# Optimization experiments

Hardware: AMD Instinct MI355X
Metric: run time of the kernel (lower is better)

## Reference

```python
import jax, jax.numpy as jnp
import numpy as np

B, T, IN_DIM, EMB = 8, 2048, 1024, 1024
NEG_INF = -1e30  # stand-in for float('-inf'); exp() underflows to 0 identically


def setup_inputs() -> dict:
    key = jax.random.key(0)
    ks = jax.random.split(key, 7)
    s = 1.0 / np.sqrt(IN_DIM)
    return {
        "x": jax.random.normal(ks[0], (B, T, IN_DIM), dtype=jnp.float32),
        "Wq": jax.random.normal(ks[1], (IN_DIM, EMB), dtype=jnp.float32) * s,
        "bq": jax.random.normal(ks[2], (EMB,), dtype=jnp.float32) * 0.01,
        "Wk": jax.random.normal(ks[3], (IN_DIM, EMB), dtype=jnp.float32) * s,
        "bk": jax.random.normal(ks[4], (EMB,), dtype=jnp.float32) * 0.01,
        "Wv": jax.random.normal(ks[5], (IN_DIM, EMB), dtype=jnp.float32) * s,
        "bv": jax.random.normal(ks[6], (EMB,), dtype=jnp.float32) * 0.01,
    }


def reference(x, Wq, bq, Wk, bk, Wv, bv):
    # projections: [B, T, EMB]
    q = x @ Wq + bq
    k = x @ Wk + bk
    v = x @ Wv + bv
    scale = jnp.asarray(EMB, x.dtype) ** 0.5
    # scores: [B, T, T]
    scores = jnp.einsum("btd,bsd->bts", q, k) / scale
    Tq = scores.shape[-2]
    causal = jnp.tril(jnp.ones((Tq, Tq), dtype=bool))  # [T, T]
    scores = jnp.where(causal, scores, jnp.asarray(NEG_INF, scores.dtype))
    # Faithful to torch.vmap(softmax): per-batch GLOBAL-matrix softmax
    # (max and sum taken over the whole [T, T] matrix, not per row).
    m = jnp.max(scores, axis=(-2, -1), keepdims=True)
    e = jnp.exp(scores - m)
    w = e / jnp.sum(e, axis=(-2, -1), keepdims=True)
    # output: [B, T, EMB]
    return jnp.einsum("bts,bsd->btd", w, v)
```

## Files before the change

### kernel.cpp

```cpp
#include <hip/hip_runtime.h>
#include <stdint.h>


#define B_   8
#define T_   2048
#define DIM  1024

typedef _Float16 f16;
typedef f16   f16x8 __attribute__((ext_vector_type(8)));
typedef f16   f16x4 __attribute__((ext_vector_type(4)));
typedef float f32x4 __attribute__((ext_vector_type(4)));

typedef const __attribute__((address_space(1))) void gvoid_t;
typedef __attribute__((address_space(3))) void lvoid_t;


__device__ __forceinline__ void stage_half256(const uint16_t* __restrict__ g, int ld,
                                              uint16_t* s, int tid) {
#pragma unroll
  for (int j = 0; j < 2; ++j) {
    int r   = j * 64 + (tid >> 3);
    int seg = (tid & 7) ^ (r & 7);
    const uint16_t* gp = g + (size_t)r * ld + seg * 8;
    uint16_t* sp = s + j * 4096 + (tid >> 6) * 512;
    __builtin_amdgcn_global_load_lds((gvoid_t*)gp, (lvoid_t*)sp, 16, 0, 0);
  }
}

__device__ __forceinline__ f16x8 frag64(const uint16_t* s, int r, int gseg) {
  return *(const f16x8*)(s + r * 64 + ((gseg ^ (r & 7)) * 8));
}

__device__ __forceinline__ void lda4(const uint16_t* s, int rbase, int quad, int l15,
                                     f16x8 o[4][2]) {
#pragma unroll
  for (int mf = 0; mf < 4; ++mf) {
    int r = rbase + mf * 16 + l15;
#pragma unroll
    for (int kk = 0; kk < 2; ++kk) o[mf][kk] = frag64(s, r, kk * 4 + quad);
  }
}

__device__ __forceinline__ void ldb2(const uint16_t* s, int rbase, int quad, int l15,
                                     f16x8 o[2][2]) {
#pragma unroll
  for (int nf = 0; nf < 2; ++nf) {
    int r = rbase + nf * 16 + l15;
#pragma unroll
    for (int kk = 0; kk < 2; ++kk) o[nf][kk] = frag64(s, r, kk * 4 + quad);
  }
}

template <int M0, int N0>
__device__ __forceinline__ void mm16(f16x8 a[4][2], f16x8 b[2][2], f32x4 (&acc)[8][4]) {
#pragma unroll
  for (int kk = 0; kk < 2; ++kk)
#pragma unroll
    for (int mf = 0; mf < 4; ++mf)
#pragma unroll
      for (int nf = 0; nf < 2; ++nf)
        acc[M0 + mf][N0 + nf] = __builtin_amdgcn_mfma_f32_16x16x32_f16(
            a[mf][kk], b[nf][kk], acc[M0 + mf][N0 + nf], 0, 0, 0);
}

#define SYNC_MFMA(AA, BB, M0, N0)                      \
  __builtin_amdgcn_s_barrier();                        \
  asm volatile("s_waitcnt lgkmcnt(0)" ::: "memory");   \
  __builtin_amdgcn_s_setprio(1);                       \
  mm16<M0, N0>(AA, BB, acc);                           \
  __builtin_amdgcn_s_setprio(0);                       \
  __builtin_amdgcn_s_barrier();

__device__ __forceinline__ void gemm256_8ph(const uint16_t* __restrict__ gA,
                                            const uint16_t* __restrict__ gB,
                                            int lda, int ldb, int nIter,
                                            uint16_t* smem, f32x4 (&acc)[8][4]) {
  const int tid = threadIdx.x, lane = tid & 63, wv = tid >> 6;
  const int quad = lane >> 4, l15 = lane & 15;
  const int wr = wv >> 2, wc = wv & 3;

  uint16_t* sA0 = smem;
  uint16_t* sA1 = smem + 16384;
  uint16_t* sB0 = smem + 32768;
  uint16_t* sB1 = smem + 49152;

  stage_half256(gA,                        lda, sA0,        tid);
  stage_half256(gA + 128 * (size_t)lda,    lda, sA0 + 8192, tid);
  stage_half256(gB,                        ldb, sB0,        tid);
  stage_half256(gB + 128 * (size_t)ldb,    ldb, sB0 + 8192, tid);
  stage_half256(gB + 64,                   ldb, sB1,        tid);
  stage_half256(gB + 64 + 128 * (size_t)ldb, ldb, sB1 + 8192, tid);
  asm volatile("s_waitcnt vmcnt(4)" ::: "memory");
  __builtin_amdgcn_s_barrier();

  f16x8 alo[4][2], ahi[4][2], blo[2][2], bhi[2][2];
  const int tmax = 2 * nIter - 1;
#pragma unroll 1
  for (int it = 0; it < nIter; ++it) {
    const int t1 = 2 * it + 1;
    int t2 = 2 * it + 2; if (t2 > tmax) t2 = tmax;
    int t3 = 2 * it + 3; if (t3 > tmax) t3 = tmax;
    const uint16_t* gA1 = gA + t1 * 64;
    const uint16_t* gA2 = gA + t2 * 64;
    const uint16_t* gB2 = gB + t2 * 64;
    const uint16_t* gB3 = gB + t3 * 64;

    lda4(sA0, wr * 128,      quad, l15, alo);
    ldb2(sB0, wc * 64,       quad, l15, blo);
    stage_half256(gA1, lda, sA1, tid);
    SYNC_MFMA(alo, blo, 0, 0)
    ldb2(sB0, wc * 64 + 32,  quad, l15, bhi);
    stage_half256(gA1 + 128 * (size_t)lda, lda, sA1 + 8192, tid);
    SYNC_MFMA(alo, bhi, 0, 2)
    lda4(sA0, wr * 128 + 64, quad, l15, ahi);
    stage_half256(gB2, ldb, sB0, tid);
    SYNC_MFMA(ahi, bhi, 4, 2)
    stage_half256(gB2 + 128 * (size_t)ldb, ldb, sB0 + 8192, tid);
    asm volatile("s_waitcnt vmcnt(4)" ::: "memory");
    SYNC_MFMA(ahi, blo, 4, 0)
    lda4(sA1, wr * 128,      quad, l15, alo);
    ldb2(sB1, wc * 64,       quad, l15, blo);
    stage_half256(gA2, lda, sA0, tid);
    SYNC_MFMA(alo, blo, 0, 0)
    ldb2(sB1, wc * 64 + 32,  quad, l15, bhi);
    stage_half256(gA2 + 128 * (size_t)lda, lda, sA0 + 8192, tid);
    SYNC_MFMA(alo, bhi, 0, 2)
    lda4(sA1, wr * 128 + 64, quad, l15, ahi);
    stage_half256(gB3, ldb, sB1, tid);
    SYNC_MFMA(ahi, bhi, 4, 2)
    stage_half256(gB3 + 128 * (size_t)ldb, ldb, sB1 + 8192, tid);
    asm volatile("s_waitcnt vmcnt(4)" ::: "memory");
    SYNC_MFMA(ahi, blo, 4, 0)
  }
}

__device__ __forceinline__ void zero_acc8(f32x4 (&acc)[8][4]) {
  f32x4 z = {0.f, 0.f, 0.f, 0.f};
#pragma unroll
  for (int i = 0; i < 8; ++i)
#pragma unroll
    for (int j = 0; j < 4; ++j) acc[i][j] = z;
}


__global__ void zero_lrow_kernel(float* __restrict__ lrow) {
  lrow[blockIdx.x * 256 + threadIdx.x] = 0.f;
}

__global__ void conv_x_kernel(const float* __restrict__ x, f16* __restrict__ xf) {
  size_t i = (size_t)blockIdx.x * 256 + threadIdx.x;
  float4 v = ((const float4*)x)[i];
  f16x4 o = {(f16)v.x, (f16)v.y, (f16)v.z, (f16)v.w};
  ((f16x4*)xf)[i] = o;
}

__global__ void convT_w_kernel(const float* __restrict__ Wq, const float* __restrict__ Wk,
                               const float* __restrict__ Wv, f16* __restrict__ WT) {
  __shared__ float tile[64][65];
  const int z = blockIdx.z;
  const float* W = (z == 0) ? Wq : (z == 1) ? Wk : Wv;
  const int r0 = blockIdx.x * 64, c0 = blockIdx.y * 64, tid = threadIdx.x;
#pragma unroll
  for (int i = 0; i < 16; ++i) {
    int rr = (tid >> 6) + 4 * i, cc = tid & 63;
    tile[rr][cc] = W[(size_t)(r0 + rr) * DIM + c0 + cc];
  }
  __syncthreads();
#pragma unroll
  for (int i = 0; i < 16; ++i) {
    int nn = (tid >> 6) + 4 * i, kk = tid & 63;
    WT[(size_t)z * DIM * DIM + (size_t)(c0 + nn) * DIM + r0 + kk] = (f16)tile[kk][nn];
  }
}

__global__ void reduce_z_kernel(const float* __restrict__ lrow, float* __restrict__ invZ) {
  const int b = blockIdx.x, tid = threadIdx.x;
  float s = 0.f;
  for (int i = tid; i < T_; i += 256) s += lrow[(size_t)b * T_ + i];
#pragma unroll
  for (int off = 1; off < 64; off <<= 1) s += __shfl_xor(s, off, 64);
  __shared__ float red[4];
  if ((tid & 63) == 0) red[tid >> 6] = s;
  __syncthreads();
  if (tid == 0) invZ[b] = 1.0f / (red[0] + red[1] + red[2] + red[3]);
}


__global__ __launch_bounds__(512, 2) void proj_kernel(
    const f16* __restrict__ xf, const f16* __restrict__ WT,
    const float* __restrict__ bq, const float* __restrict__ bk, const float* __restrict__ bv,
    f16* __restrict__ q, f16* __restrict__ k, f16* __restrict__ vT) {
  __shared__ uint16_t smem[65536];

  const int bid = blockIdx.x;
  const int xcd = bid & 7, local = bid >> 3;
  const int bx = xcd * 8 + (local & 7);
  const int zy = local >> 3;
  const int z = zy >> 2, by = zy & 3;
  const size_t arow = (size_t)bx * 256;
  const int    bcol = by * 256;

  f32x4 acc[8][4];
  zero_acc8(acc);
  gemm256_8ph((const uint16_t*)xf + arow * DIM,
              (const uint16_t*)WT + (size_t)z * DIM * DIM + (size_t)bcol * DIM,
              DIM, DIM, 8, smem, acc);

  const float* bias = (z == 0) ? bq : (z == 1) ? bk : bv;
  const int tid = threadIdx.x, lane = tid & 63, wv = tid >> 6;
  const int quad = lane >> 4, l15 = lane & 15;
  const int wr = wv >> 2, wc = wv & 3;
  if (z < 2) {
    f16* O = z ? k : q;
#pragma unroll
    for (int mf = 0; mf < 8; ++mf)
#pragma unroll
      for (int nf = 0; nf < 4; ++nf) {
        int n = bcol + wc * 64 + nf * 16 + l15;
        float bb = bias[n];
        size_t row0 = arow + wr * 128 + mf * 16 + quad * 4;
#pragma unroll
        for (int r = 0; r < 4; ++r)
          O[(row0 + r) * DIM + n] = (f16)(acc[mf][nf][r] + bb);
      }
  } else {
#pragma unroll
    for (int mf = 0; mf < 8; ++mf)
#pragma unroll
      for (int nf = 0; nf < 4; ++nf) {
        int n = bcol + wc * 64 + nf * 16 + l15;
        float bb = bias[n];
        int row0 = (int)arow + wr * 128 + mf * 16 + quad * 4;
        int bb_i = row0 >> 11, t0 = row0 & 2047;
        f16x4 pk;
#pragma unroll
        for (int r = 0; r < 4; ++r) pk[r] = (f16)(acc[mf][nf][r] + bb);
        *(f16x4*)(vT + ((size_t)bb_i * DIM + n) * T_ + t0) = pk;
      }
  }
}

__global__ __launch_bounds__(512, 2) void scores_kernel(
    const f16* __restrict__ q, const f16* __restrict__ k,
    f16* __restrict__ E, float* __restrict__ lrow) {
  __shared__ uint16_t smem[65536];
  const int bid = blockIdx.x;
  const int b = bid & 7, tri = bid >> 3;
  int qi = 0;
  while ((qi + 1) * (qi + 2) / 2 <= tri) ++qi;
  const int ki = tri - qi * (qi + 1) / 2;

  f32x4 acc[8][4];
  zero_acc8(acc);
  gemm256_8ph((const uint16_t*)(q + ((size_t)b * T_ + qi * 256) * DIM),
              (const uint16_t*)(k + ((size_t)b * T_ + ki * 256) * DIM),
              DIM, DIM, 8, smem, acc);

  const int tid = threadIdx.x, lane = tid & 63, wv = tid >> 6;
  const int quad = lane >> 4, l15 = lane & 15;
  const int wr = wv >> 2, wc = wv & 3;
  f16*   Eb = E + (size_t)b * T_ * T_;
  float* lb = lrow + (size_t)b * T_;
  const bool diag = (ki == qi);
#pragma unroll
  for (int mf = 0; mf < 8; ++mf) {
    float rs[4] = {0.f, 0.f, 0.f, 0.f};
#pragma unroll
    for (int nf = 0; nf < 4; ++nf)
#pragma unroll
      for (int r = 0; r < 4; ++r) {
        int t = qi * 256 + wr * 128 + mf * 16 + quad * 4 + r;
        int s = ki * 256 + wc * 64 + nf * 16 + l15;
        float e = 0.f;
        if (!diag || s <= t) e = __expf(fminf(acc[mf][nf][r] * 0.03125f, 11.f));
        Eb[(size_t)t * T_ + s] = (f16)e;
        rs[r] += e;
      }
#pragma unroll
    for (int off = 1; off < 16; off <<= 1)
#pragma unroll
      for (int r = 0; r < 4; ++r) rs[r] += __shfl_xor(rs[r], off, 64);
    if (l15 == 0)
#pragma unroll
      for (int r = 0; r < 4; ++r)
        atomicAdd(&lb[qi * 256 + wr * 128 + mf * 16 + quad * 4 + r], rs[r]);
  }
}

__global__ __launch_bounds__(512, 2) void pv_kernel(
    const f16* __restrict__ E, const f16* __restrict__ vT,
    const float* __restrict__ invZ, float* __restrict__ out) {
  __shared__ uint16_t smem[65536];
  const int bid = blockIdx.x;
  const int b = bid & 7, local = bid >> 3;
  const int qi = local & 7, nt = local >> 3;

  f32x4 acc[8][4];
  zero_acc8(acc);
  gemm256_8ph((const uint16_t*)(E + ((size_t)b * T_ + qi * 256) * (size_t)T_),
              (const uint16_t*)(vT + ((size_t)b * DIM + nt * 256) * (size_t)T_),
              T_, T_, (qi + 1) * 2, smem, acc);

  const float iz = invZ[b];
  const int tid = threadIdx.x, lane = tid & 63, wv = tid >> 6;
  const int quad = lane >> 4, l15 = lane & 15;
  const int wr = wv >> 2, wc = wv & 3;
  float* ob = out + (size_t)b * T_ * DIM;
#pragma unroll
  for (int mf = 0; mf < 8; ++mf)
#pragma unroll
    for (int nf = 0; nf < 4; ++nf)
#pragma unroll
      for (int r = 0; r < 4; ++r) {
        int t = qi * 256 + wr * 128 + mf * 16 + quad * 4 + r;
        int n = nt * 256 + wc * 64 + nf * 16 + l15;
        ob[(size_t)t * DIM + n] = acc[mf][nf][r] * iz;
      }
}


extern "C" void kernel_launch(void* const* d_in, const int* in_sizes, int n_in,
                              void* d_out, int out_size, void* d_ws, size_t ws_size,
                              hipStream_t stream) {
  const float* x  = (const float*)d_in[0];
  const float* Wq = (const float*)d_in[1];
  const float* bq = (const float*)d_in[2];
  const float* Wk = (const float*)d_in[3];
  const float* bk = (const float*)d_in[4];
  const float* Wv = (const float*)d_in[5];
  const float* bv = (const float*)d_in[6];
  float* out = (float*)d_out;

  char* ws = (char*)d_ws;
  f16*   E    = (f16*)ws;
  f16*   xf   = (f16*)ws;
  f16*   q    = (f16*)(ws + 67108864);
  f16*   k    = (f16*)(ws + 100663296);
  f16*   vT   = (f16*)(ws + 134217728);
  f16*   WT   = (f16*)(ws + 167772160);
  float* lrow = (float*)(ws + 174063616);
  float* invZ = (float*)(ws + 174129152);
  if (ws_size < (size_t)174129184) return;

  zero_lrow_kernel<<<64, 256, 0, stream>>>(lrow);
  conv_x_kernel<<<16384, 256, 0, stream>>>(x, xf);
  convT_w_kernel<<<dim3(16, 16, 3), 256, 0, stream>>>(Wq, Wk, Wv, WT);
  proj_kernel<<<dim3(768), 512, 0, stream>>>(xf, WT, bq, bk, bv, q, k, vT);
  scores_kernel<<<dim3(288), 512, 0, stream>>>(q, k, E, lrow);
  reduce_z_kernel<<<B_, 256, 0, stream>>>(lrow, invZ);
  pv_kernel<<<dim3(256), 512, 0, stream>>>(E, vT, invZ, out);
}
```

Baseline: 353.5 us.

## Rebalance causal PV GEMM with 256x128 tiles and paired query blocks

The PV kernel now uses 256x128 output tiles instead of 256x256, and each block processes two query tiles (qi and 7-qi). This evens out the triangular causal workload across blocks and lowers LDS use per block. The GEMM main loop also peels its last iteration, so the clamped redundant prefetch loads are gone. The costs are a smaller N tile, which means less reuse of A loads, and a serial loop of two GEMMs inside each block.

```diff
diff --git a/kernel.cpp b/kernel.cpp
--- a/kernel.cpp
+++ b/kernel.cpp
@@ -51,6 +51,13 @@
   }
 }
 
+__device__ __forceinline__ void ldb1(const uint16_t* s, int rbase, int quad, int l15,
+                                     f16x8 o[2]) {
+  int r = rbase + l15;
+#pragma unroll
+  for (int kk = 0; kk < 2; ++kk) o[kk] = frag64(s, r, kk * 4 + quad);
+}
+
 template <int M0, int N0>
 __device__ __forceinline__ void mm16(f16x8 a[4][2], f16x8 b[2][2], f32x4 (&acc)[8][4]) {
 #pragma unroll
@@ -61,6 +68,16 @@
       for (int nf = 0; nf < 2; ++nf)
         acc[M0 + mf][N0 + nf] = __builtin_amdgcn_mfma_f32_16x16x32_f16(
             a[mf][kk], b[nf][kk], acc[M0 + mf][N0 + nf], 0, 0, 0);
+}
+
+template <int M0, int N0>
+__device__ __forceinline__ void mm8(f16x8 a[4][2], f16x8 b[2], f32x4 (&acc)[8][2]) {
+#pragma unroll
+  for (int kk = 0; kk < 2; ++kk)
+#pragma unroll
+    for (int mf = 0; mf < 4; ++mf)
+      acc[M0 + mf][N0] = __builtin_amdgcn_mfma_f32_16x16x32_f16(
+          a[mf][kk], b[kk], acc[M0 + mf][N0], 0, 0, 0);
 }
 
 #define SYNC_MFMA(AA, BB, M0, N0)                      \
@@ -71,35 +88,40 @@
   __builtin_amdgcn_s_setprio(0);                       \
   __builtin_amdgcn_s_barrier();
 
+#define SYNC_MFMA8(AA, BB, M0, N0)                     \
+  __builtin_amdgcn_s_barrier();                        \
+  asm volatile("s_waitcnt lgkmcnt(0)" ::: "memory");   \
+  __builtin_amdgcn_s_setprio(1);                       \
+  mm8<M0, N0>(AA, BB, acc);                            \
+  __builtin_amdgcn_s_setprio(0);                       \
+  __builtin_amdgcn_s_barrier();
+
 __device__ __forceinline__ void gemm256_8ph(const uint16_t* __restrict__ gA,
                                             const uint16_t* __restrict__ gB,
                                             int lda, int ldb, int nIter,
                                             uint16_t* smem, f32x4 (&acc)[8][4]) {
-  const int tid = threadIdx.x, lane = tid & 63, wv = tid >> 6;
+  const int tid = threadIdx.x, lane = tid & 63;
   const int quad = lane >> 4, l15 = lane & 15;
-  const int wr = wv >> 2, wc = wv & 3;
+  const int wv = tid >> 6, wr = wv >> 2, wc = wv & 3;
 
   uint16_t* sA0 = smem;
   uint16_t* sA1 = smem + 16384;
   uint16_t* sB0 = smem + 32768;
   uint16_t* sB1 = smem + 49152;
 
-  stage_half256(gA,                        lda, sA0,        tid);
-  stage_half256(gA + 128 * (size_t)lda,    lda, sA0 + 8192, tid);
-  stage_half256(gB,                        ldb, sB0,        tid);
-  stage_half256(gB + 128 * (size_t)ldb,    ldb, sB0 + 8192, tid);
-  stage_half256(gB + 64,                   ldb, sB1,        tid);
+  stage_half256(gA,                          lda, sA0,        tid);
+  stage_half256(gA + 128 * (size_t)lda,      lda, sA0 + 8192, tid);
+  stage_half256(gB,                          ldb, sB0,        tid);
+  stage_half256(gB + 128 * (size_t)ldb,      ldb, sB0 + 8192, tid);
+  stage_half256(gB + 64,                     ldb, sB1,        tid);
   stage_half256(gB + 64 + 128 * (size_t)ldb, ldb, sB1 + 8192, tid);
   asm volatile("s_waitcnt vmcnt(4)" ::: "memory");
   __builtin_amdgcn_s_barrier();
 
   f16x8 alo[4][2], ahi[4][2], blo[2][2], bhi[2][2];
-  const int tmax = 2 * nIter - 1;
 #pragma unroll 1
-  for (int it = 0; it < nIter; ++it) {
-    const int t1 = 2 * it + 1;
-    int t2 = 2 * it + 2; if (t2 > tmax) t2 = tmax;
-    int t3 = 2 * it + 3; if (t3 > tmax) t3 = tmax;
+  for (int it = 0; it < nIter - 1; ++it) {
+    const int t1 = 2 * it + 1, t2 = 2 * it + 2, t3 = 2 * it + 3;
     const uint16_t* gA1 = gA + t1 * 64;
     const uint16_t* gA2 = gA + t2 * 64;
     const uint16_t* gB2 = gB + t2 * 64;
@@ -132,6 +154,106 @@
     asm volatile("s_waitcnt vmcnt(4)" ::: "memory");
     SYNC_MFMA(ahi, blo, 4, 0)
   }
+
+  {
+    const uint16_t* gA1 = gA + (2 * nIter - 1) * 64;
+    lda4(sA0, wr * 128,      quad, l15, alo);
+    ldb2(sB0, wc * 64,       quad, l15, blo);
+    stage_half256(gA1, lda, sA1, tid);
+    SYNC_MFMA(alo, blo, 0, 0)
+    ldb2(sB0, wc * 64 + 32,  quad, l15, bhi);
+    stage_half256(gA1 + 128 * (size_t)lda, lda, sA1 + 8192, tid);
+    SYNC_MFMA(alo, bhi, 0, 2)
+    lda4(sA0, wr * 128 + 64, quad, l15, ahi);
+    SYNC_MFMA(ahi, bhi, 4, 2)
+    asm volatile("s_waitcnt vmcnt(0)" ::: "memory");
+    SYNC_MFMA(ahi, blo, 4, 0)
+    lda4(sA1, wr * 128,      quad, l15, alo);
+    ldb2(sB1, wc * 64,       quad, l15, blo);
+    SYNC_MFMA(alo, blo, 0, 0)
+    ldb2(sB1, wc * 64 + 32,  quad, l15, bhi);
+    SYNC_MFMA(alo, bhi, 0, 2)
+    lda4(sA1, wr * 128 + 64, quad, l15, ahi);
+    SYNC_MFMA(ahi, bhi, 4, 2)
+    SYNC_MFMA(ahi, blo, 4, 0)
+  }
+}
+
+__device__ __forceinline__ void gemm256n128_8ph(const uint16_t* __restrict__ gA,
+                                                const uint16_t* __restrict__ gB,
+                                                int lda, int ldb, int nIter,
+                                                uint16_t* smem, f32x4 (&acc)[8][2]) {
+  const int tid = threadIdx.x, lane = tid & 63;
+  const int quad = lane >> 4, l15 = lane & 15;
+  const int wv = tid >> 6, wr = wv >> 2, wc = wv & 3;
+
+  uint16_t* sA0 = smem;
+  uint16_t* sA1 = smem + 16384;
+  uint16_t* sB0 = smem + 32768;
+  uint16_t* sB1 = smem + 40960;
+
+  stage_half256(gA,                     lda, sA0,        tid);
+  stage_half256(gA + 128 * (size_t)lda, lda, sA0 + 8192, tid);
+  stage_half256(gB,                     ldb, sB0,        tid);
+  stage_half256(gB + 64,                ldb, sB1,        tid);
+  asm volatile("s_waitcnt vmcnt(2)" ::: "memory");
+  __builtin_amdgcn_s_barrier();
+
+  f16x8 alo[4][2], ahi[4][2], b0[2], b1[2];
+#pragma unroll 1
+  for (int it = 0; it < nIter - 1; ++it) {
+    const int t1 = 2 * it + 1, t2 = 2 * it + 2, t3 = 2 * it + 3;
+    const uint16_t* gA1 = gA + t1 * 64;
+    const uint16_t* gA2 = gA + t2 * 64;
+
+    lda4(sA0, wr * 128,      quad, l15, alo);
+    ldb1(sB0, wc * 32,       quad, l15, b0);
+    stage_half256(gA1, lda, sA1, tid);
+    SYNC_MFMA8(alo, b0, 0, 0)
+    ldb1(sB0, wc * 32 + 16,  quad, l15, b1);
+    stage_half256(gA1 + 128 * (size_t)lda, lda, sA1 + 8192, tid);
+    SYNC_MFMA8(alo, b1, 0, 1)
+    lda4(sA0, wr * 128 + 64, quad, l15, ahi);
+    stage_half256(gB + t2 * 64, ldb, sB0, tid);
+    SYNC_MFMA8(ahi, b1, 4, 1)
+    asm volatile("s_waitcnt vmcnt(2)" ::: "memory");
+    SYNC_MFMA8(ahi, b0, 4, 0)
+    lda4(sA1, wr * 128,      quad, l15, alo);
+    ldb1(sB1, wc * 32,       quad, l15, b0);
+    stage_half256(gA2, lda, sA0, tid);
+    SYNC_MFMA8(alo, b0, 0, 0)
+    ldb1(sB1, wc * 32 + 16,  quad, l15, b1);
+    stage_half256(gA2 + 128 * (size_t)lda, lda, sA0 + 8192, tid);
+    SYNC_MFMA8(alo, b1, 0, 1)
+    lda4(sA1, wr * 128 + 64, quad, l15, ahi);
+    stage_half256(gB + t3 * 64, ldb, sB1, tid);
+    SYNC_MFMA8(ahi, b1, 4, 1)
+    asm volatile("s_waitcnt vmcnt(2)" ::: "memory");
+    SYNC_MFMA8(ahi, b0, 4, 0)
+  }
+
+  {
+    const uint16_t* gA1 = gA + (2 * nIter - 1) * 64;
+    lda4(sA0, wr * 128,      quad, l15, alo);
+    ldb1(sB0, wc * 32,       quad, l15, b0);
+    stage_half256(gA1, lda, sA1, tid);
+    SYNC_MFMA8(alo, b0, 0, 0)
+    ldb1(sB0, wc * 32 + 16,  quad, l15, b1);
+    stage_half256(gA1 + 128 * (size_t)lda, lda, sA1 + 8192, tid);
+    SYNC_MFMA8(alo, b1, 0, 1)
+    lda4(sA0, wr * 128 + 64, quad, l15, ahi);
+    SYNC_MFMA8(ahi, b1, 4, 1)
+    asm volatile("s_waitcnt vmcnt(0)" ::: "memory");
+    SYNC_MFMA8(ahi, b0, 4, 0)
+    lda4(sA1, wr * 128,      quad, l15, alo);
+    ldb1(sB1, wc * 32,       quad, l15, b0);
+    SYNC_MFMA8(alo, b0, 0, 0)
+    ldb1(sB1, wc * 32 + 16,  quad, l15, b1);
+    SYNC_MFMA8(alo, b1, 0, 1)
+    lda4(sA1, wr * 128 + 64, quad, l15, ahi);
+    SYNC_MFMA8(ahi, b1, 4, 1)
+    SYNC_MFMA8(ahi, b0, 4, 0)
+  }
 }
 
 __device__ __forceinline__ void zero_acc8(f32x4 (&acc)[8][4]) {
@@ -290,32 +412,40 @@
 __global__ __launch_bounds__(512, 2) void pv_kernel(
     const f16* __restrict__ E, const f16* __restrict__ vT,
     const float* __restrict__ invZ, float* __restrict__ out) {
-  __shared__ uint16_t smem[65536];
+  __shared__ uint16_t smem[49152];
   const int bid = blockIdx.x;
   const int b = bid & 7, local = bid >> 3;
-  const int qi = local & 7, nt = local >> 3;
-
-  f32x4 acc[8][4];
-  zero_acc8(acc);
-  gemm256_8ph((const uint16_t*)(E + ((size_t)b * T_ + qi * 256) * (size_t)T_),
-              (const uint16_t*)(vT + ((size_t)b * DIM + nt * 256) * (size_t)T_),
-              T_, T_, (qi + 1) * 2, smem, acc);
+  const int nt = local & 7, pair = local >> 3;
 
   const float iz = invZ[b];
   const int tid = threadIdx.x, lane = tid & 63, wv = tid >> 6;
   const int quad = lane >> 4, l15 = lane & 15;
   const int wr = wv >> 2, wc = wv & 3;
   float* ob = out + (size_t)b * T_ * DIM;
-#pragma unroll
-  for (int mf = 0; mf < 8; ++mf)
-#pragma unroll
-    for (int nf = 0; nf < 4; ++nf)
-#pragma unroll
-      for (int r = 0; r < 4; ++r) {
-        int t = qi * 256 + wr * 128 + mf * 16 + quad * 4 + r;
-        int n = nt * 256 + wc * 64 + nf * 16 + l15;
-        ob[(size_t)t * DIM + n] = acc[mf][nf][r] * iz;
-      }
+  const uint16_t* Bv = (const uint16_t*)(vT + ((size_t)b * DIM + nt * 128) * (size_t)T_);
+
+#pragma unroll 1
+  for (int j = 0; j < 2; ++j) {
+    const int qi = j ? (7 - pair) : pair;
+    f32x4 acc[8][2];
+    {
+      f32x4 z = {0.f, 0.f, 0.f, 0.f};
+#pragma unroll
+      for (int i = 0; i < 8; ++i) { acc[i][0] = z; acc[i][1] = z; }
+    }
+    gemm256n128_8ph((const uint16_t*)(E + ((size_t)b * T_ + qi * 256) * (size_t)T_),
+                    Bv, T_, T_, (qi + 1) * 2, smem, acc);
+#pragma unroll
+    for (int mf = 0; mf < 8; ++mf)
+#pragma unroll
+      for (int nf = 0; nf < 2; ++nf)
+#pragma unroll
+        for (int r = 0; r < 4; ++r) {
+          int t = qi * 256 + wr * 128 + mf * 16 + quad * 4 + r;
+          int n = nt * 128 + wc * 32 + nf * 16 + l15;
+          ob[(size_t)t * DIM + n] = acc[mf][nf][r] * iz;
+        }
+  }
 }
 
 
```

Measured after the change: 346.7 us. Within noise of the previous version (-1.9%).
